# Kernel optimization log

Measured on AMD Instinct MI355X. Metric: run time of the kernel, lower is better.

Reference implementation:

```python
import jax, jax.numpy as jnp
import numpy as np

QMIN, QMAX = -128.0, 127.0
SMALL_SCALE_THRESHOLD = 6.1e-05


def quant_kernel(x):
    # x: [M, K] float32 -> per-row scale (f32), zero point (i32), precomputed sum (i32), q (i8)
    rmin = jnp.minimum(jnp.min(x, axis=1), 0.0).astype(jnp.float32)
    rmax = jnp.maximum(jnp.max(x, axis=1), 0.0).astype(jnp.float32)
    scale = (rmax - rmin) / (QMAX - QMIN)
    # faithful replication of `scale == 0.0 + isinf(1/scale)` (precedence: 0.0 + bool)
    isinf = jnp.isinf(1.0 / scale)
    scale = jnp.where(scale == (0.0 + isinf.astype(jnp.float32)), 0.1, scale)
    small = scale < SMALL_SCALE_THRESHOLD
    amp = SMALL_SCALE_THRESHOLD / scale
    scale = jnp.where(small, SMALL_SCALE_THRESHOLD, scale)
    rmax = jnp.where(small, amp * rmax, rmax)
    rmin = jnp.where(small, amp * rmin, rmin)
    zp_from_min = QMIN - rmin / scale
    zp_from_max = QMAX - rmax / scale
    err_min = abs(QMIN) + jnp.abs(rmin / scale)
    err_max = abs(QMAX) + jnp.abs(rmax / scale)
    zp0 = jnp.where(err_min < err_max, zp_from_min, zp_from_max)
    zp = jnp.round(zp0).astype(jnp.int32)
    zp = jnp.where(zp0 < QMIN, jnp.int32(QMIN), zp)
    zp = jnp.where(zp0 > QMAX, jnp.int32(QMAX), zp)
    inv = 1.0 / scale
    sums = jnp.round(jnp.sum(x, axis=1) * inv).astype(jnp.int32)
    t = jnp.round(x * inv[:, None]) + zp[:, None].astype(jnp.float32)
    q = jnp.clip(t, QMIN, QMAX).astype(jnp.int8)
    return scale, zp, sums, q


def dequant_kernel(d, bias, m1_scales, m1_zeros, m1_sums, m2_scales, m2_zeros, m2_sums):
    # d: [M, N] int32 raw GEMM; m1_*: [M, 1]; m2_*: [1, N]
    temp = (m1_zeros * m2_sums).astype(jnp.int32) + (m1_sums * m2_zeros).astype(jnp.int32)
    scale = m1_scales * m2_scales
    return bias + ((d - temp).astype(jnp.float32) * scale).astype(bias.dtype)


def setup_inputs() -> dict:
    key = jax.random.key(0)
    k1, k2, k3, k4, k5 = jax.random.split(key, 5)
    B, S, K, N = 4, 4096, 1024, 1024
    inp = jax.random.normal(k1, (B, S, K), dtype=jnp.float32)
    qweight = jax.random.randint(k2, (N, K), -128, 128, dtype=jnp.int32).astype(jnp.int8)
    bias = jax.random.normal(k3, (N,), dtype=jnp.float32)
    w_scales = (jax.random.uniform(k4, (N,), dtype=jnp.float32) * 0.01 + 1e-3)
    w_zeros = jax.random.randint(k5, (N,), -10, 10, dtype=jnp.int32)
    # consistent precomputed weight sums (sum of quantized vals minus K*zero)
    w_sums = (jnp.sum(qweight.astype(jnp.int32), axis=1) - K * w_zeros).astype(jnp.int32)
    return {"inp": inp, "qweight": qweight, "bias": bias,
            "w_scales": w_scales, "w_zeros": w_zeros, "w_sums": w_sums}


def reference(inp, qweight, bias, w_scales, w_zeros, w_sums):
    B, S, K = inp.shape
    x = inp.reshape(B * S, K)
    scales, zeros, sums, qinp = quant_kernel(x)
    # int8 GEMM accumulated in int32: [M, K] @ [K, N]
    d = jnp.matmul(qinp.astype(jnp.int32), qweight.T.astype(jnp.int32))
    M, N = d.shape
    out = dequant_kernel(d, bias, scales.reshape(M, 1), zeros.reshape(M, 1),
                         sums.reshape(M, 1), w_scales.reshape(1, N),
                         w_zeros.reshape(1, N), w_sums.reshape(1, N))
    return out.reshape(B, S, N)
```

## Files before the change

kernel.cpp:

```cpp
#include <hip/hip_runtime.h>
#include <cstdint>
#include <cstddef>

typedef int v4i __attribute__((ext_vector_type(4)));

#define QMIN_F (-128.0f)
#define QMAX_F (127.0f)
#define SMALL_THR 6.1e-05f

#define WAITVM(n) asm volatile("s_waitcnt vmcnt(" #n ")" ::: "memory")

__global__ __launch_bounds__(256) void pack_w_kernel(
    const int* __restrict__ w32, int* __restrict__ w8, int n4) {
  int i = blockIdx.x * blockDim.x + threadIdx.x;
  if (i >= n4) return;
  v4i v = *(const v4i*)(w32 + i * 4);
  w8[i] = (v.x & 255) | ((v.y & 255) << 8) | ((v.z & 255) << 16) | (v.w << 24);
}

__global__ __launch_bounds__(256) void quant_rows_kernel(
    const float* __restrict__ x, signed char* __restrict__ q,
    float* __restrict__ scales, int* __restrict__ zps, int* __restrict__ sums,
    int K) {
  const int wave = threadIdx.x >> 6;
  const int lane = threadIdx.x & 63;
  const int row  = blockIdx.x * 4 + wave;
  const float* xr = x + (size_t)row * K;

  float4 v[4];
  float vmin = 0.0f, vmax = 0.0f, vsum = 0.0f;
#pragma unroll
  for (int j = 0; j < 4; ++j) {
    v[j] = *(const float4*)(xr + j * 256 + lane * 4);
    vmin = fminf(vmin, fminf(fminf(v[j].x, v[j].y), fminf(v[j].z, v[j].w)));
    vmax = fmaxf(vmax, fmaxf(fmaxf(v[j].x, v[j].y), fmaxf(v[j].z, v[j].w)));
    vsum += (v[j].x + v[j].y) + (v[j].z + v[j].w);
  }
#pragma unroll
  for (int off = 32; off >= 1; off >>= 1) {
    vmin = fminf(vmin, __shfl_xor(vmin, off));
    vmax = fmaxf(vmax, __shfl_xor(vmax, off));
    vsum += __shfl_xor(vsum, off);
  }

  float scale = (vmax - vmin) / (QMAX_F - QMIN_F);
  float isinf_f = isinf(1.0f / scale) ? 1.0f : 0.0f;
  if (scale == isinf_f) scale = 0.1f;
  float rmin = vmin, rmax = vmax;
  if (scale < SMALL_THR) {
    float amp = SMALL_THR / scale;
    scale = SMALL_THR;
    rmax *= amp;
    rmin *= amp;
  }
  float rdmin = rmin / scale, rdmax = rmax / scale;
  float err_min = 128.0f + fabsf(rdmin);
  float err_max = 127.0f + fabsf(rdmax);
  float zp0 = (err_min < err_max) ? (QMIN_F - rdmin) : (QMAX_F - rdmax);
  int zp = (int)rintf(zp0);
  if (zp0 < QMIN_F) zp = -128;
  if (zp0 > QMAX_F) zp = 127;
  float inv = 1.0f / scale;

  if (lane == 0) {
    scales[row] = scale;
    zps[row]    = zp;
    sums[row]   = (int)rintf(vsum * inv);
  }

  const float zpf = (float)zp;
  int* qi = (int*)(q + (size_t)row * K);
#pragma unroll
  for (int j = 0; j < 4; ++j) {
    float t0 = fminf(fmaxf(rintf(v[j].x * inv) + zpf, QMIN_F), QMAX_F);
    float t1 = fminf(fmaxf(rintf(v[j].y * inv) + zpf, QMIN_F), QMAX_F);
    float t2 = fminf(fmaxf(rintf(v[j].z * inv) + zpf, QMIN_F), QMAX_F);
    float t3 = fminf(fmaxf(rintf(v[j].w * inv) + zpf, QMIN_F), QMAX_F);
    int pack = ((int)t0 & 255) | (((int)t1 & 255) << 8) |
               (((int)t2 & 255) << 16) | ((int)t3 << 24);
    qi[j * 64 + lane] = pack;
  }
}

__device__ __forceinline__ void gload_lds16(const void* g, void* l) {
  __builtin_amdgcn_global_load_lds(
      (const __attribute__((address_space(1))) void*)g,
      (__attribute__((address_space(3))) void*)l, 16, 0, 0);
}

__device__ __forceinline__ void stage_tile(
    const signed char* __restrict__ q, const signed char* __restrict__ w,
    char* bufA, char* bufB, int rowA0, int rowB0, int k0, int K, int tid) {
#pragma unroll
  for (int i = 0; i < 2; ++i) {
    int c  = (i << 9) + tid;
    int r  = c >> 2;
    int sl = (c & 3) ^ ((r >> 1) & 3);
    gload_lds16(q + (size_t)(rowA0 + r) * K + k0 + (sl << 4), bufA + (c << 4));
  }
#pragma unroll
  for (int i = 0; i < 2; ++i) {
    int c  = (i << 9) + tid;
    int r  = c >> 2;
    int sl = (c & 3) ^ ((r >> 1) & 3);
    gload_lds16(w + (size_t)(rowB0 + r) * K + k0 + (sl << 4), bufB + (c << 4));
  }
}

__global__ __launch_bounds__(512, 2) void gemm_dequant_kernel(
    const signed char* __restrict__ q, const signed char* __restrict__ w,
    const float* __restrict__ scales, const int* __restrict__ zps,
    const int* __restrict__ sums, const float* __restrict__ bias,
    const float* __restrict__ w_scales, const int* __restrict__ w_zeros,
    const int* __restrict__ w_sums, float* __restrict__ out,
    int N, int K, int nblk) {
  __shared__ char sh[3][32768];
  const int tid  = threadIdx.x;
  const int lane = tid & 63;
  const int wave = tid >> 6;
  const int wr = wave >> 2;
  const int wc = wave & 3;
  const int fr = lane & 15;
  const int kb = lane >> 4;
  const int ntN = N >> 8;
  const int per = nblk >> 3;
  const int lin = ((int)blockIdx.x & 7) * per + ((int)blockIdx.x >> 3);
  const int rowA0 = (lin / ntN) << 8;
  const int rowB0 = (lin % ntN) << 8;
  const int wrbase = wr << 7;
  const int wcbase = wc << 6;

  v4i acc[8][4];
#pragma unroll
  for (int i = 0; i < 8; ++i)
#pragma unroll
    for (int j = 0; j < 4; ++j) {
      v4i z = {0, 0, 0, 0};
      acc[i][j] = z;
    }

  const int NT = K >> 6;
  stage_tile(q, w, sh[0], sh[0] + 16384, rowA0, rowB0, 0, K, tid);
  stage_tile(q, w, sh[1], sh[1] + 16384, rowA0, rowB0, 64, K, tid);

  for (int t = 0; t < NT; ++t) {
    if (t + 2 < NT) {
      int b = (t + 2) % 3;
      stage_tile(q, w, sh[b], sh[b] + 16384, rowA0, rowB0, (t + 2) << 6, K, tid);
    }
    if (t < NT - 2)      { WAITVM(8); }
    else if (t == NT - 2){ WAITVM(4); }
    else                 { WAITVM(0); }
    __builtin_amdgcn_s_barrier();

    const char* bA = sh[t % 3];
    const char* bB = bA + 16384;

    v4i bfrag[4], afrag[4];
#pragma unroll
    for (int n = 0; n < 4; ++n) {
      int rb = wcbase + (n << 4) + fr;
      bfrag[n] = *(const v4i*)(bB + (rb << 6) + ((kb ^ ((rb >> 1) & 3)) << 4));
    }
#pragma unroll
    for (int m = 0; m < 4; ++m) {
      int ra = wrbase + (m << 4) + fr;
      afrag[m] = *(const v4i*)(bA + (ra << 6) + ((kb ^ ((ra >> 1) & 3)) << 4));
    }
    __builtin_amdgcn_s_barrier();
    __builtin_amdgcn_s_setprio(1);
#pragma unroll
    for (int m = 0; m < 4; ++m)
#pragma unroll
      for (int n = 0; n < 4; ++n)
        acc[m][n] = __builtin_amdgcn_mfma_i32_16x16x64_i8(afrag[m], bfrag[n],
                                                          acc[m][n], 0, 0, 0);
    __builtin_amdgcn_s_setprio(0);
#pragma unroll
    for (int m = 0; m < 4; ++m) {
      int ra = wrbase + ((m + 4) << 4) + fr;
      afrag[m] = *(const v4i*)(bA + (ra << 6) + ((kb ^ ((ra >> 1) & 3)) << 4));
    }
    __builtin_amdgcn_s_barrier();
    __builtin_amdgcn_s_setprio(1);
#pragma unroll
    for (int m = 0; m < 4; ++m)
#pragma unroll
      for (int n = 0; n < 4; ++n)
        acc[m + 4][n] = __builtin_amdgcn_mfma_i32_16x16x64_i8(
            afrag[m], bfrag[n], acc[m + 4][n], 0, 0, 0);
    __builtin_amdgcn_s_setprio(0);
    asm volatile("" ::: "memory");
    __builtin_amdgcn_s_barrier();
  }

  const int baseM = rowA0 + wrbase;
  const int baseN = rowB0 + wcbase;
  const int qr = (lane >> 4) << 2;
  const int qc = lane & 15;
  float cb[4], cwsc[4];
  int cwz[4], cws[4];
#pragma unroll
  for (int n = 0; n < 4; ++n) {
    int col = baseN + (n << 4) + qc;
    cb[n]   = bias[col];
    cwsc[n] = w_scales[col];
    cwz[n]  = w_zeros[col];
    cws[n]  = w_sums[col];
  }
#pragma unroll
  for (int i = 0; i < 8; ++i) {
    const int m0 = baseM + (i << 4) + qr;
    float sc[4];
    int zp4[4], sm4[4];
#pragma unroll
    for (int j = 0; j < 4; ++j) {
      sc[j]  = scales[m0 + j];
      zp4[j] = zps[m0 + j];
      sm4[j] = sums[m0 + j];
    }
#pragma unroll
    for (int n = 0; n < 4; ++n) {
      const int col = baseN + (n << 4) + qc;
#pragma unroll
      for (int j = 0; j < 4; ++j) {
        int d    = acc[i][n][j];
        int temp = zp4[j] * cws[n] + sm4[j] * cwz[n];
        out[(size_t)(m0 + j) * N + col] = cb[n] + (float)(d - temp) * (sc[j] * cwsc[n]);
      }
    }
  }
}

extern "C" void kernel_launch(void* const* d_in, const int* in_sizes, int n_in,
                              void* d_out, int out_size, void* d_ws, size_t ws_size,
                              hipStream_t stream) {
  const float* inp      = (const float*)d_in[0];
  const int*   qw32     = (const int*)d_in[1];
  const float* bias     = (const float*)d_in[2];
  const float* w_scales = (const float*)d_in[3];
  const int*   w_zeros  = (const int*)d_in[4];
  const int*   w_sums   = (const int*)d_in[5];

  const int N = in_sizes[2];
  const int K = in_sizes[1] / N;
  const int M = in_sizes[0] / K;

  float*       scales = (float*)d_ws;
  int*         zps    = (int*)((char*)d_ws + (size_t)M * 4);
  int*         sums   = (int*)((char*)d_ws + (size_t)M * 8);
  signed char* q      = (signed char*)((char*)d_ws + (size_t)M * 12);
  signed char* w8     = (signed char*)((char*)d_ws + (size_t)M * 12 + (size_t)M * K);

  const int n4 = (N * K) / 4;
  const int nblk = (M / 256) * (N / 256);
  pack_w_kernel<<<(n4 + 255) / 256, 256, 0, stream>>>(qw32, (int*)w8, n4);
  quant_rows_kernel<<<M / 4, 256, 0, stream>>>(inp, q, scales, zps, sums, K);
  gemm_dequant_kernel<<<nblk, 512, 0, stream>>>(
      q, w8, scales, zps, sums, bias, w_scales, w_zeros, w_sums,
      (float*)d_out, N, K, nblk);
}
```

Baseline: 51.16 us.

## Shrink GEMM tile to 128x256, double-buffer, fuse weight packing into quant

Folds the weight int32-to-int8 packing into the row-quantization kernel, removing one kernel launch. The GEMM block tile shrinks from 256x256 to 128x256 and the LDS ring goes from three buffers to two, which cuts per-block LDS and registers so launch bounds can allow 4 blocks per CU and the grid doubles. One inner barrier and the second MFMA half are dropped, and outputs are written with nontemporal stores. In exchange, each block reuses less data per staged tile and prefetch depth drops from two tiles to one, which may expose more memory latency.

```diff
diff --git a/kernel.cpp b/kernel.cpp
--- a/kernel.cpp
+++ b/kernel.cpp
@@ -10,18 +10,17 @@
 
 #define WAITVM(n) asm volatile("s_waitcnt vmcnt(" #n ")" ::: "memory")
 
-__global__ __launch_bounds__(256) void pack_w_kernel(
-    const int* __restrict__ w32, int* __restrict__ w8, int n4) {
-  int i = blockIdx.x * blockDim.x + threadIdx.x;
-  if (i >= n4) return;
-  v4i v = *(const v4i*)(w32 + i * 4);
-  w8[i] = (v.x & 255) | ((v.y & 255) << 8) | ((v.z & 255) << 16) | (v.w << 24);
-}
-
 __global__ __launch_bounds__(256) void quant_rows_kernel(
     const float* __restrict__ x, signed char* __restrict__ q,
     float* __restrict__ scales, int* __restrict__ zps, int* __restrict__ sums,
-    int K) {
+    const int* __restrict__ w32, int* __restrict__ w8pk, int n4, int K) {
+  const int gidx = blockIdx.x * 256 + threadIdx.x;
+  if (gidx < n4) {
+    v4i pv = *(const v4i*)(w32 + gidx * 4);
+    w8pk[gidx] = (pv.x & 255) | ((pv.y & 255) << 8) | ((pv.z & 255) << 16) |
+                 (pv.w << 24);
+  }
+
   const int wave = threadIdx.x >> 6;
   const int lane = threadIdx.x & 63;
   const int row  = blockIdx.x * 4 + wave;
@@ -88,33 +87,36 @@
       (__attribute__((address_space(3))) void*)l, 16, 0, 0);
 }
 
+#define BUFA_SZ 8192
+#define BUFB_SZ 16384
+
 __device__ __forceinline__ void stage_tile(
     const signed char* __restrict__ q, const signed char* __restrict__ w,
-    char* bufA, char* bufB, int rowA0, int rowB0, int k0, int K, int tid) {
+    char* buf, int rowA0, int rowB0, int k0, int K, int tid) {
+  {
+    int c  = tid;
+    int r  = c >> 2;
+    int sl = (c & 3) ^ ((r >> 1) & 3);
+    gload_lds16(q + (size_t)(rowA0 + r) * K + k0 + (sl << 4), buf + (c << 4));
+  }
 #pragma unroll
   for (int i = 0; i < 2; ++i) {
     int c  = (i << 9) + tid;
     int r  = c >> 2;
     int sl = (c & 3) ^ ((r >> 1) & 3);
-    gload_lds16(q + (size_t)(rowA0 + r) * K + k0 + (sl << 4), bufA + (c << 4));
-  }
-#pragma unroll
-  for (int i = 0; i < 2; ++i) {
-    int c  = (i << 9) + tid;
-    int r  = c >> 2;
-    int sl = (c & 3) ^ ((r >> 1) & 3);
-    gload_lds16(w + (size_t)(rowB0 + r) * K + k0 + (sl << 4), bufB + (c << 4));
-  }
-}
-
-__global__ __launch_bounds__(512, 2) void gemm_dequant_kernel(
+    gload_lds16(w + (size_t)(rowB0 + r) * K + k0 + (sl << 4),
+                buf + BUFA_SZ + (c << 4));
+  }
+}
+
+__global__ __launch_bounds__(512, 4) void gemm_dequant_kernel(
     const signed char* __restrict__ q, const signed char* __restrict__ w,
     const float* __restrict__ scales, const int* __restrict__ zps,
     const int* __restrict__ sums, const float* __restrict__ bias,
     const float* __restrict__ w_scales, const int* __restrict__ w_zeros,
     const int* __restrict__ w_sums, float* __restrict__ out,
     int N, int K, int nblk) {
-  __shared__ char sh[3][32768];
+  __shared__ char sh[2][BUFA_SZ + BUFB_SZ];
   const int tid  = threadIdx.x;
   const int lane = tid & 63;
   const int wave = tid >> 6;
@@ -125,14 +127,14 @@
   const int ntN = N >> 8;
   const int per = nblk >> 3;
   const int lin = ((int)blockIdx.x & 7) * per + ((int)blockIdx.x >> 3);
-  const int rowA0 = (lin / ntN) << 8;
+  const int rowA0 = (lin / ntN) << 7;
   const int rowB0 = (lin % ntN) << 8;
-  const int wrbase = wr << 7;
+  const int wrbase = wr << 6;
   const int wcbase = wc << 6;
 
-  v4i acc[8][4];
-#pragma unroll
-  for (int i = 0; i < 8; ++i)
+  v4i acc[4][4];
+#pragma unroll
+  for (int i = 0; i < 4; ++i)
 #pragma unroll
     for (int j = 0; j < 4; ++j) {
       v4i z = {0, 0, 0, 0};
@@ -140,23 +142,21 @@
     }
 
   const int NT = K >> 6;
-  stage_tile(q, w, sh[0], sh[0] + 16384, rowA0, rowB0, 0, K, tid);
-  stage_tile(q, w, sh[1], sh[1] + 16384, rowA0, rowB0, 64, K, tid);
+  stage_tile(q, w, sh[0], rowA0, rowB0, 0, K, tid);
 
   for (int t = 0; t < NT; ++t) {
-    if (t + 2 < NT) {
-      int b = (t + 2) % 3;
-      stage_tile(q, w, sh[b], sh[b] + 16384, rowA0, rowB0, (t + 2) << 6, K, tid);
-    }
-    if (t < NT - 2)      { WAITVM(8); }
-    else if (t == NT - 2){ WAITVM(4); }
-    else                 { WAITVM(0); }
+    if (t + 1 < NT) {
+      stage_tile(q, w, sh[(t + 1) & 1], rowA0, rowB0, (t + 1) << 6, K, tid);
+      WAITVM(3);
+    } else {
+      WAITVM(0);
+    }
     __builtin_amdgcn_s_barrier();
 
-    const char* bA = sh[t % 3];
-    const char* bB = bA + 16384;
-
-    v4i bfrag[4], afrag[4];
+    const char* bA = sh[t & 1];
+    const char* bB = bA + BUFA_SZ;
+
+    v4i afrag[4], bfrag[4];
 #pragma unroll
     for (int n = 0; n < 4; ++n) {
       int rb = wcbase + (n << 4) + fr;
@@ -167,7 +167,6 @@
       int ra = wrbase + (m << 4) + fr;
       afrag[m] = *(const v4i*)(bA + (ra << 6) + ((kb ^ ((ra >> 1) & 3)) << 4));
     }
-    __builtin_amdgcn_s_barrier();
     __builtin_amdgcn_s_setprio(1);
 #pragma unroll
     for (int m = 0; m < 4; ++m)
@@ -175,20 +174,6 @@
       for (int n = 0; n < 4; ++n)
         acc[m][n] = __builtin_amdgcn_mfma_i32_16x16x64_i8(afrag[m], bfrag[n],
                                                           acc[m][n], 0, 0, 0);
-    __builtin_amdgcn_s_setprio(0);
-#pragma unroll
-    for (int m = 0; m < 4; ++m) {
-      int ra = wrbase + ((m + 4) << 4) + fr;
-      afrag[m] = *(const v4i*)(bA + (ra << 6) + ((kb ^ ((ra >> 1) & 3)) << 4));
-    }
-    __builtin_amdgcn_s_barrier();
-    __builtin_amdgcn_s_setprio(1);
-#pragma unroll
-    for (int m = 0; m < 4; ++m)
-#pragma unroll
-      for (int n = 0; n < 4; ++n)
-        acc[m + 4][n] = __builtin_amdgcn_mfma_i32_16x16x64_i8(
-            afrag[m], bfrag[n], acc[m + 4][n], 0, 0, 0);
     __builtin_amdgcn_s_setprio(0);
     asm volatile("" ::: "memory");
     __builtin_amdgcn_s_barrier();
@@ -209,7 +194,7 @@
     cws[n]  = w_sums[col];
   }
 #pragma unroll
-  for (int i = 0; i < 8; ++i) {
+  for (int i = 0; i < 4; ++i) {
     const int m0 = baseM + (i << 4) + qr;
     float sc[4];
     int zp4[4], sm4[4];
@@ -226,7 +211,8 @@
       for (int j = 0; j < 4; ++j) {
         int d    = acc[i][n][j];
         int temp = zp4[j] * cws[n] + sm4[j] * cwz[n];
-        out[(size_t)(m0 + j) * N + col] = cb[n] + (float)(d - temp) * (sc[j] * cwsc[n]);
+        float val = cb[n] + (float)(d - temp) * (sc[j] * cwsc[n]);
+        __builtin_nontemporal_store(val, &out[(size_t)(m0 + j) * N + col]);
       }
     }
   }
@@ -253,9 +239,9 @@
   signed char* w8     = (signed char*)((char*)d_ws + (size_t)M * 12 + (size_t)M * K);
 
   const int n4 = (N * K) / 4;
-  const int nblk = (M / 256) * (N / 256);
-  pack_w_kernel<<<(n4 + 255) / 256, 256, 0, stream>>>(qw32, (int*)w8, n4);
-  quant_rows_kernel<<<M / 4, 256, 0, stream>>>(inp, q, scales, zps, sums, K);
+  const int nblk = (M / 128) * (N / 256);
+  quant_rows_kernel<<<M / 4, 256, 0, stream>>>(inp, q, scales, zps, sums,
+                                               qw32, (int*)w8, n4, K);
   gemm_dequant_kernel<<<nblk, 512, 0, stream>>>(
       q, w8, scales, zps, sums, bias, w_scales, w_zeros, w_sums,
       (float*)d_out, N, K, nblk);
```

Result: no change. 52.09 us (+1.8%).
